# Kernel tuning notes

Measured on AMD Instinct MI355X. Metric: run time of the kernel, lower is better.

The kernel has to match this reference:

```python
import jax, jax.numpy as jnp
import numpy as np

B, N, C, K = 32, 4096, 768, 64

def setup_inputs() -> dict:
    key = jax.random.key(0)
    k1, k2 = jax.random.split(key)
    x = jax.random.normal(k1, (B, N, C), dtype=jnp.float32)
    # nn.Linear(in_dim, K, bias=False) weight has shape [K, in_dim]
    W = jax.random.normal(k2, (K, C), dtype=jnp.float32) * (1.0 / np.sqrt(C))
    return {"x_bhwc": x, "W": W}

def reference(x_bhwc, W):
    # logits: [B, N, K]
    logits = jnp.einsum('bnc,kc->bnk', x_bhwc, W)
    # softmax over spatial dim N (dim=1)
    attn = jax.nn.softmax(logits, axis=1)
    # weighted sum over N -> [B, K, C]
    tokens = jnp.einsum('bnk,bnc->bkc', attn, x_bhwc)
    return tokens
```

## Files before the change

### kernel.cpp

```cpp
#include <hip/hip_runtime.h>
#include <hip/hip_bf16.h>

#define Bdim 32
#define Ndim 4096
#define Cdim 768
#define Kdim 64

typedef float f32x4 __attribute__((ext_vector_type(4)));
typedef short s16x8 __attribute__((ext_vector_type(8)));
typedef __bf16 bf16x8 __attribute__((ext_vector_type(8)));

__device__ __forceinline__ short f2bf(float f) {
  return __builtin_bit_cast(short, (__bf16)f);
}
__device__ __forceinline__ float bf2f(short s) {
  return (float)__builtin_bit_cast(__bf16, s);
}
__device__ __forceinline__ f32x4 MFMA(s16x8 a, s16x8 b, f32x4 c) {
  return __builtin_amdgcn_mfma_f32_16x16x32_bf16(
      __builtin_bit_cast(bf16x8, a), __builtin_bit_cast(bf16x8, b), c, 0, 0, 0);
}

__global__ void k0_wcvt(const float* __restrict__ W, short* __restrict__ Wr) {
  int idx = blockIdx.x * 256 + threadIdx.x;
  if (idx >= Kdim * Cdim / 8) return;
  int k = idx / (Cdim / 8), c8 = idx % (Cdim / 8);
  int cs = c8 >> 2, g = c8 & 3;
  int t = k >> 4, i = k & 15;
  const float* src = W + (size_t)k * Cdim + c8 * 8;
  s16x8 v;
#pragma unroll
  for (int e = 0; e < 8; ++e) v[e] = f2bf(src[e]);
  *(s16x8*)(Wr + ((((size_t)cs * 4 + t) * 4 + g) * 16 + i) * 8) = v;
}

__global__ __launch_bounds__(256) void k1_logits(
    const float* __restrict__ x, const short* __restrict__ Wr,
    short* __restrict__ Lx, float* __restrict__ pm, float* __restrict__ ps) {
  const int blk = blockIdx.x;
  const int b = blk >> 6;
  const int ntile = blk & 63;
  const int tid = threadIdx.x;
  const int w = tid >> 6;
  const int l = tid & 63;
  const int g = l >> 4, i = l & 15;

  const float* xrow = x + (size_t)(b * Ndim + ntile * 64 + w * 16 + i) * Cdim;
  f32x4 acc[4] = {};
  f32x4 xv[2][8];
  s16x8 wv[2][4];

#pragma unroll
  for (int s = 0; s < 4; ++s) {
    const f32x4* ap = (const f32x4*)(xrow + g * 8 + s * 32);
    xv[0][2 * s] = ap[0];
    xv[0][2 * s + 1] = ap[1];
  }
#pragma unroll
  for (int t = 0; t < 4; ++t)
    wv[0][t] = *(const s16x8*)(Wr + (((size_t)t * 4 + g) * 16 + i) * 8);

#pragma unroll
  for (int grp = 0; grp < 6; ++grp) {
    const int cur = grp & 1, nxt = cur ^ 1;
    if (grp < 5) {
#pragma unroll
      for (int s = 0; s < 4; ++s) {
        const f32x4* ap = (const f32x4*)(xrow + (grp + 1) * 128 + g * 8 + s * 32);
        xv[nxt][2 * s] = ap[0];
        xv[nxt][2 * s + 1] = ap[1];
      }
    }
#pragma unroll
    for (int s = 0; s < 4; ++s) {
      const int wcur = s & 1, wnxt = wcur ^ 1;
      if (s < 3 || grp < 5) {
        const int gg = (s < 3) ? grp : grp + 1;
        const int ss = (s < 3) ? s + 1 : 0;
#pragma unroll
        for (int t = 0; t < 4; ++t)
          wv[wnxt][t] = *(const s16x8*)(
              Wr + ((((size_t)(gg * 4 + ss) * 4 + t) * 4 + g) * 16 + i) * 8);
      }
      s16x8 af;
#pragma unroll
      for (int e = 0; e < 4; ++e) af[e] = f2bf(xv[cur][2 * s][e]);
#pragma unroll
      for (int e = 0; e < 4; ++e) af[4 + e] = f2bf(xv[cur][2 * s + 1][e]);
#pragma unroll
      for (int t = 0; t < 4; ++t) acc[t] = MFMA(af, wv[wcur][t], acc[t]);
    }
  }

  short* Lb = Lx + (size_t)b * (Ndim * Kdim);
  float rnd[4][4];
#pragma unroll
  for (int t = 0; t < 4; ++t) {
#pragma unroll
    for (int r = 0; r < 4; ++r) {
      int n = ntile * 64 + w * 16 + g * 4 + r;
      int k = t * 16 + i;
      short hv = f2bf(acc[t][r]);
      Lb[(n >> 3) * 512 + k * 8 + (n & 7)] = hv;
      rnd[t][r] = bf2f(hv);
    }
  }

  __shared__ float rm[4][4][16], rs[4][4][16];
  float tm[4];
#pragma unroll
  for (int t = 0; t < 4; ++t) {
    tm[t] = fmaxf(fmaxf(rnd[t][0], rnd[t][1]), fmaxf(rnd[t][2], rnd[t][3]));
    tm[t] = fmaxf(tm[t], __shfl_xor(tm[t], 16));
    tm[t] = fmaxf(tm[t], __shfl_xor(tm[t], 32));
  }
  if (g == 0) {
#pragma unroll
    for (int t = 0; t < 4; ++t) rm[w][t][i] = tm[t];
  }
  __syncthreads();
  float M[4], sv[4];
#pragma unroll
  for (int t = 0; t < 4; ++t) {
    M[t] = fmaxf(fmaxf(rm[0][t][i], rm[1][t][i]), fmaxf(rm[2][t][i], rm[3][t][i]));
    sv[t] = __expf(rnd[t][0] - M[t]) + __expf(rnd[t][1] - M[t]) +
            __expf(rnd[t][2] - M[t]) + __expf(rnd[t][3] - M[t]);
    sv[t] += __shfl_xor(sv[t], 16);
    sv[t] += __shfl_xor(sv[t], 32);
  }
  if (g == 0) {
#pragma unroll
    for (int t = 0; t < 4; ++t) rs[w][t][i] = sv[t];
  }
  __syncthreads();
  if (w == 0 && g == 0) {
#pragma unroll
    for (int t = 0; t < 4; ++t) {
      float S = rs[0][t][i] + rs[1][t][i] + rs[2][t][i] + rs[3][t][i];
      pm[((size_t)b * 64 + ntile) * 64 + t * 16 + i] = M[t];
      ps[((size_t)b * 64 + ntile) * 64 + t * 16 + i] = S;
    }
  }
}

__global__ __launch_bounds__(256) void k2b_combine(
    const float* __restrict__ pm, const float* __restrict__ ps,
    float* __restrict__ mout, float* __restrict__ invd) {
  const int b = blockIdx.x;
  const int t = threadIdx.x;
  const int k = t & 63, nt4 = t >> 6;
  float am[16];
  float M = -1e30f;
#pragma unroll
  for (int j = 0; j < 16; ++j) {
    am[j] = pm[((size_t)b * 64 + nt4 * 16 + j) * 64 + k];
    M = fmaxf(M, am[j]);
  }
  __shared__ float sm[4][64], ss[4][64];
  sm[nt4][k] = M;
  __syncthreads();
  M = fmaxf(fmaxf(sm[0][k], sm[1][k]), fmaxf(sm[2][k], sm[3][k]));
  float S = 0.f;
#pragma unroll
  for (int j = 0; j < 16; ++j)
    S += ps[((size_t)b * 64 + nt4 * 16 + j) * 64 + k] * __expf(am[j] - M);
  ss[nt4][k] = S;
  __syncthreads();
  if (nt4 == 0) {
    float St = ss[0][k] + ss[1][k] + ss[2][k] + ss[3][k];
    mout[b * 64 + k] = M;
    invd[b * 64 + k] = 1.f / St;
  }
}

__global__ __launch_bounds__(256) void k2c_pexp(
    const short* __restrict__ Lx, const float* __restrict__ mv,
    const float* __restrict__ invd, short* __restrict__ P) {
  const int u = blockIdx.x * 256 + threadIdx.x;
  const int k = u & 63, b = u >> 15;
  s16x8 v = *(const s16x8*)(Lx + (size_t)u * 8);
  const float m = mv[(b << 6) + k];
  const float sc = invd[(b << 6) + k];
  s16x8 o;
#pragma unroll
  for (int e = 0; e < 8; ++e) o[e] = f2bf(sc * __expf(bf2f(v[e]) - m));
  *(s16x8*)(P + (size_t)u * 8) = o;
}

#define CT 48
#define NCH 128
#define NQ 4
__device__ __forceinline__ int swz(int c) {
  return ((((c >> 3) ^ c) & 7) << 4);
}
__global__ __launch_bounds__(256) void k3_tokens(
    const float* __restrict__ x, const short* __restrict__ P,
    float* __restrict__ part) {
  __shared__ short xs[CT * 128];
  char* xsb = (char*)xs;
  const int blk = blockIdx.x;
  const int q = blk & 3;
  const int ct = (blk >> 2) & 15;
  const int b = blk >> 6;
  const int tid = threadIdx.x;
  const int w = tid >> 6, l = tid & 63, g = l >> 4, i = l & 15;

  const float* xb = x + (size_t)b * Ndim * Cdim;
  const short* Pb = P + (size_t)b * (Ndim * Kdim);

  f32x4 acc[3] = {};

#define LOADX(ch, buf)                                                        \
  do {                                                                        \
    const int n0_ = (ch) * NCH;                                               \
    _Pragma("unroll") for (int uu = 0; uu < 3; ++uu) {                        \
      int u_ = tid + uu * 256;                                                \
      int n_ = u_ / 6, c8_ = u_ % 6;                                          \
      const f32x4* src_ =                                                     \
          (const f32x4*)(xb + (size_t)(n0_ + n_) * Cdim + ct * CT + c8_ * 8); \
      buf[uu][0] = src_[0];                                                   \
      buf[uu][1] = src_[1];                                                   \
    }                                                                         \
  } while (0)

#define LOADL(ch, lvb)                                                        \
  do {                                                                        \
    const int nb8_ = (ch) * 16;                                               \
    _Pragma("unroll") for (int ns = 0; ns < 4; ++ns) {                        \
      lvb[ns] = *(const s16x8*)(Pb + (size_t)(nb8_ + ns * 4 + g) * 512 +      \
                                (w * 16 + i) * 8);                            \
    }                                                                         \
  } while (0)

#define STORELDS(buf)                                                         \
  do {                                                                        \
    _Pragma("unroll") for (int uu = 0; uu < 3; ++uu) {                        \
      int u_ = tid + uu * 256;                                                \
      int n_ = u_ / 6, c8_ = u_ % 6;                                          \
      _Pragma("unroll") for (int e = 0; e < 8; ++e) {                         \
        int c_ = c8_ * 8 + e;                                                 \
        float fv_ = (e < 4) ? buf[uu][0][e] : buf[uu][1][e - 4];              \
        *(short*)(xsb + c_ * 256 + ((2 * n_) ^ swz(c_))) = f2bf(fv_);         \
      }                                                                       \
    }                                                                         \
  } while (0)

#define COMPUTE(lvb)                                                          \
  do {                                                                        \
    _Pragma("unroll") for (int ns = 0; ns < 4; ++ns) {                        \
      _Pragma("unroll") for (int cs = 0; cs < 3; ++cs) {                      \
        const int c_ = cs * 16 + i;                                           \
        s16x8 bfr_ = *(const s16x8*)(xsb + c_ * 256 +                         \
                                     ((ns * 64 + g * 16) ^ swz(c_)));         \
        acc[cs] = MFMA(lvb[ns], bfr_, acc[cs]);                               \
      }                                                                       \
    }                                                                         \
  } while (0)

  f32x4 stA[3][2], stB[3][2];
  s16x8 lvA[4], lvB[4];

  const int ch0 = q * 8;
  LOADX(ch0, stA);
  LOADL(ch0, lvA);
  for (int ch = 0; ch < 8; ch += 2) {
    __syncthreads();
    STORELDS(stA);
    LOADX(ch0 + ch + 1, stB);
    LOADL(ch0 + ch + 1, lvB);
    __syncthreads();
    COMPUTE(lvA);
    __syncthreads();
    STORELDS(stB);
    if (ch + 2 < 8) {
      LOADX(ch0 + ch + 2, stA);
      LOADL(ch0 + ch + 2, lvA);
    }
    __syncthreads();
    COMPUTE(lvB);
  }

  float* pb = part + ((size_t)q * Bdim + b) * (Kdim * Cdim);
#pragma unroll
  for (int r = 0; r < 4; ++r) {
    const int k = w * 16 + g * 4 + r;
#pragma unroll
    for (int cs = 0; cs < 3; ++cs) {
      pb[(size_t)k * Cdim + ct * CT + cs * 16 + i] = acc[cs][r];
    }
  }
#undef LOADX
#undef LOADL
#undef STORELDS
#undef COMPUTE
}

#define QSTRIDE (Bdim * Kdim * Cdim / 4)
__global__ __launch_bounds__(256) void k4_reduce(
    const float* __restrict__ part, float* __restrict__ out) {
  const int idx = blockIdx.x * 256 + threadIdx.x;
  const f32x4* p = (const f32x4*)part;
  f32x4 s = p[idx] + p[idx + QSTRIDE] + p[idx + 2 * QSTRIDE] + p[idx + 3 * QSTRIDE];
  ((f32x4*)out)[idx] = s;
}

extern "C" void kernel_launch(void* const* d_in, const int* in_sizes, int n_in,
                              void* d_out, int out_size, void* d_ws, size_t ws_size,
                              hipStream_t stream) {
  const float* x = (const float*)d_in[0];
  const float* W = (const float*)d_in[1];
  float* out = (float*)d_out;
  char* ws = (char*)d_ws;

  short* Wb = (short*)ws;
  short* Lx = (short*)(ws + (1 << 17));
  char* after = ws + (1 << 17) + (size_t)Bdim * Ndim * Kdim * 2;
  float* pm = (float*)after;
  float* psum = pm + Bdim * 64 * 64;
  float* mv = psum + Bdim * 64 * 64;
  float* iv = mv + Bdim * Kdim;
  float* part = iv + Bdim * Kdim;
  short* P = (short*)(part + 4 * Bdim * Kdim * Cdim);

  hipLaunchKernelGGL(k0_wcvt, dim3(24), dim3(256), 0, stream, W, Wb);
  hipLaunchKernelGGL(k1_logits, dim3(Bdim * 64), dim3(256), 0, stream, x, Wb, Lx, pm, psum);
  hipLaunchKernelGGL(k2b_combine, dim3(Bdim), dim3(256), 0, stream, pm, psum, mv, iv);
  hipLaunchKernelGGL(k2c_pexp, dim3(Bdim * Ndim * Kdim / 8 / 256), dim3(256), 0, stream,
                     Lx, mv, iv, P);
  hipLaunchKernelGGL(k3_tokens, dim3(Bdim * 16 * NQ), dim3(256), 0, stream, x, P, part);
  hipLaunchKernelGGL(k4_reduce, dim3(Bdim * Kdim * Cdim / 4 / 256), dim3(256), 0, stream,
                     part, out);
}
```

Measured before the change: 227.1 us.

## Emit bf16 copy of x in logits kernel and read it in tokens kernel

The logits kernel now writes the bf16-converted x rows it already builds for the MFMA into a workspace buffer, and loads fp32 x with nontemporal hints. The tokens kernel reads this bf16 copy instead of re-reading and converting fp32 x, halving its input bytes and removing its conversion work. The exp kernel now writes P in place over the logits buffer, which frees the workspace slot used for the bf16 copy. Total DRAM traffic stays about the same (an extra bf16 write in exchange for a cheaper second read), so any benefit depends on that write staying in cache and on the removed conversion work.

```diff
diff --git a/kernel.cpp b/kernel.cpp
--- a/kernel.cpp
+++ b/kernel.cpp
@@ -36,7 +36,8 @@
 
 __global__ __launch_bounds__(256) void k1_logits(
     const float* __restrict__ x, const short* __restrict__ Wr,
-    short* __restrict__ Lx, float* __restrict__ pm, float* __restrict__ ps) {
+    short* __restrict__ Lx, short* __restrict__ xb16,
+    float* __restrict__ pm, float* __restrict__ ps) {
   const int blk = blockIdx.x;
   const int b = blk >> 6;
   const int ntile = blk & 63;
@@ -45,7 +46,9 @@
   const int l = tid & 63;
   const int g = l >> 4, i = l & 15;
 
-  const float* xrow = x + (size_t)(b * Ndim + ntile * 64 + w * 16 + i) * Cdim;
+  const int row = b * Ndim + ntile * 64 + w * 16 + i;
+  const float* xrow = x + (size_t)row * Cdim;
+  short* brow = xb16 + (size_t)row * Cdim;
   f32x4 acc[4] = {};
   f32x4 xv[2][8];
   s16x8 wv[2][4];
@@ -53,8 +56,8 @@
 #pragma unroll
   for (int s = 0; s < 4; ++s) {
     const f32x4* ap = (const f32x4*)(xrow + g * 8 + s * 32);
-    xv[0][2 * s] = ap[0];
-    xv[0][2 * s + 1] = ap[1];
+    xv[0][2 * s] = __builtin_nontemporal_load(ap);
+    xv[0][2 * s + 1] = __builtin_nontemporal_load(ap + 1);
   }
 #pragma unroll
   for (int t = 0; t < 4; ++t)
@@ -67,8 +70,8 @@
 #pragma unroll
       for (int s = 0; s < 4; ++s) {
         const f32x4* ap = (const f32x4*)(xrow + (grp + 1) * 128 + g * 8 + s * 32);
-        xv[nxt][2 * s] = ap[0];
-        xv[nxt][2 * s + 1] = ap[1];
+        xv[nxt][2 * s] = __builtin_nontemporal_load(ap);
+        xv[nxt][2 * s + 1] = __builtin_nontemporal_load(ap + 1);
       }
     }
 #pragma unroll
@@ -87,6 +90,7 @@
       for (int e = 0; e < 4; ++e) af[e] = f2bf(xv[cur][2 * s][e]);
 #pragma unroll
       for (int e = 0; e < 4; ++e) af[4 + e] = f2bf(xv[cur][2 * s + 1][e]);
+      *(s16x8*)(brow + grp * 128 + g * 8 + s * 32) = af;
 #pragma unroll
       for (int t = 0; t < 4; ++t) acc[t] = MFMA(af, wv[wcur][t], acc[t]);
     }
@@ -174,17 +178,17 @@
 }
 
 __global__ __launch_bounds__(256) void k2c_pexp(
-    const short* __restrict__ Lx, const float* __restrict__ mv,
-    const float* __restrict__ invd, short* __restrict__ P) {
+    short* __restrict__ LxP, const float* __restrict__ mv,
+    const float* __restrict__ invd) {
   const int u = blockIdx.x * 256 + threadIdx.x;
   const int k = u & 63, b = u >> 15;
-  s16x8 v = *(const s16x8*)(Lx + (size_t)u * 8);
+  s16x8 v = *(const s16x8*)(LxP + (size_t)u * 8);
   const float m = mv[(b << 6) + k];
   const float sc = invd[(b << 6) + k];
   s16x8 o;
 #pragma unroll
   for (int e = 0; e < 8; ++e) o[e] = f2bf(sc * __expf(bf2f(v[e]) - m));
-  *(s16x8*)(P + (size_t)u * 8) = o;
+  *(s16x8*)(LxP + (size_t)u * 8) = o;
 }
 
 #define CT 48
@@ -194,7 +198,7 @@
   return ((((c >> 3) ^ c) & 7) << 4);
 }
 __global__ __launch_bounds__(256) void k3_tokens(
-    const float* __restrict__ x, const short* __restrict__ P,
+    const short* __restrict__ xb16, const short* __restrict__ P,
     float* __restrict__ part) {
   __shared__ short xs[CT * 128];
   char* xsb = (char*)xs;
@@ -205,7 +209,7 @@
   const int tid = threadIdx.x;
   const int w = tid >> 6, l = tid & 63, g = l >> 4, i = l & 15;
 
-  const float* xb = x + (size_t)b * Ndim * Cdim;
+  const short* xb = xb16 + (size_t)b * Ndim * Cdim;
   const short* Pb = P + (size_t)b * (Ndim * Kdim);
 
   f32x4 acc[3] = {};
@@ -216,10 +220,8 @@
     _Pragma("unroll") for (int uu = 0; uu < 3; ++uu) {                        \
       int u_ = tid + uu * 256;                                                \
       int n_ = u_ / 6, c8_ = u_ % 6;                                          \
-      const f32x4* src_ =                                                     \
-          (const f32x4*)(xb + (size_t)(n0_ + n_) * Cdim + ct * CT + c8_ * 8); \
-      buf[uu][0] = src_[0];                                                   \
-      buf[uu][1] = src_[1];                                                   \
+      buf[uu] = *(const s16x8*)(xb + (size_t)(n0_ + n_) * Cdim + ct * CT +    \
+                                c8_ * 8);                                     \
     }                                                                         \
   } while (0)
 
@@ -239,8 +241,7 @@
       int n_ = u_ / 6, c8_ = u_ % 6;                                          \
       _Pragma("unroll") for (int e = 0; e < 8; ++e) {                         \
         int c_ = c8_ * 8 + e;                                                 \
-        float fv_ = (e < 4) ? buf[uu][0][e] : buf[uu][1][e - 4];              \
-        *(short*)(xsb + c_ * 256 + ((2 * n_) ^ swz(c_))) = f2bf(fv_);         \
+        *(short*)(xsb + c_ * 256 + ((2 * n_) ^ swz(c_))) = buf[uu][e];        \
       }                                                                       \
     }                                                                         \
   } while (0)
@@ -257,7 +258,7 @@
     }                                                                         \
   } while (0)
 
-  f32x4 stA[3][2], stB[3][2];
+  s16x8 stA[3], stB[3];
   s16x8 lvA[4], lvB[4];
 
   const int ch0 = q * 8;
@@ -320,14 +321,14 @@
   float* mv = psum + Bdim * 64 * 64;
   float* iv = mv + Bdim * Kdim;
   float* part = iv + Bdim * Kdim;
-  short* P = (short*)(part + 4 * Bdim * Kdim * Cdim);
+  short* xb16 = (short*)(part + 4 * Bdim * Kdim * Cdim);
 
   hipLaunchKernelGGL(k0_wcvt, dim3(24), dim3(256), 0, stream, W, Wb);
-  hipLaunchKernelGGL(k1_logits, dim3(Bdim * 64), dim3(256), 0, stream, x, Wb, Lx, pm, psum);
+  hipLaunchKernelGGL(k1_logits, dim3(Bdim * 64), dim3(256), 0, stream, x, Wb, Lx, xb16, pm, psum);
   hipLaunchKernelGGL(k2b_combine, dim3(Bdim), dim3(256), 0, stream, pm, psum, mv, iv);
   hipLaunchKernelGGL(k2c_pexp, dim3(Bdim * Ndim * Kdim / 8 / 256), dim3(256), 0, stream,
-                     Lx, mv, iv, P);
-  hipLaunchKernelGGL(k3_tokens, dim3(Bdim * 16 * NQ), dim3(256), 0, stream, x, P, part);
+                     Lx, mv, iv);
+  hipLaunchKernelGGL(k3_tokens, dim3(Bdim * 16 * NQ), dim3(256), 0, stream, xb16, Lx, part);
   hipLaunchKernelGGL(k4_reduce, dim3(Bdim * Kdim * Cdim / 4 / 256), dim3(256), 0, stream,
                      part, out);
 }
```

After: 257.2 us. +13.3%, slower.
